# Kernel tuning notes

Measured on AMD Instinct MI355X. Metric: run time of the kernel, lower is better.

Reference implementation:

```python
import jax, jax.numpy as jnp
import numpy as np

N = 50000
E = 800000
IN_DIM, HID, HEADS, OUT = 128, 32, 8, 64
NEG_SLOPE = 0.2
EPS = 1e-16


def setup_inputs() -> dict:
    key = jax.random.key(0)
    ks = jax.random.split(key, 10)
    return {
        "x": jax.random.normal(ks[0], (N, IN_DIM), dtype=jnp.float32),
        "edge_index": jax.random.randint(ks[1], (2, E), 0, N, dtype=jnp.int64)
        if jax.config.jax_enable_x64 else jax.random.randint(ks[1], (2, E), 0, N, dtype=jnp.int32),
        "W1": jax.random.normal(ks[2], (HEADS * HID, IN_DIM), dtype=jnp.float32) * 0.1,
        "att_src1": jax.random.normal(ks[3], (HEADS, HID), dtype=jnp.float32) * 0.1,
        "att_dst1": jax.random.normal(ks[4], (HEADS, HID), dtype=jnp.float32) * 0.1,
        "b1": jnp.zeros((HEADS * HID,), dtype=jnp.float32),
        "W2": jax.random.normal(ks[5], (OUT, HEADS * HID), dtype=jnp.float32) * 0.1,
        "att_src2": jax.random.normal(ks[6], (1, OUT), dtype=jnp.float32) * 0.1,
        "att_dst2": jax.random.normal(ks[7], (1, OUT), dtype=jnp.float32) * 0.1,
        "b2": jnp.zeros((OUT,), dtype=jnp.float32),
    }


def _gat_conv(x, src, dst, W, att_src, att_dst, bias, heads, out_dim, concat, n_nodes):
    # x: [N, F_in]; W: [heads*out_dim, F_in]; att_*: [heads, out_dim]
    h = (x @ W.T).reshape(n_nodes, heads, out_dim)      # [N, H, D]
    a_src = jnp.einsum('nhd,hd->nh', h, att_src)         # [N, H]
    a_dst = jnp.einsum('nhd,hd->nh', h, att_dst)
    alpha = jax.nn.leaky_relu(a_src[src] + a_dst[dst], NEG_SLOPE)  # [E, H]
    # segment softmax over edges grouped by destination node
    m = jax.ops.segment_max(alpha, dst, num_segments=n_nodes)
    alpha = jnp.exp(alpha - m[dst])
    s = jax.ops.segment_sum(alpha, dst, num_segments=n_nodes)
    alpha = alpha / (s[dst] + EPS)
    msg = h[src] * alpha[:, :, None]                     # [E, H, D]
    out = jax.ops.segment_sum(msg, dst, num_segments=n_nodes)  # [N, H, D]
    if concat:
        out = out.reshape(n_nodes, heads * out_dim)
    else:
        out = out.mean(axis=1)
    return out + bias


def reference(x, edge_index, W1, att_src1, att_dst1, b1, W2, att_src2, att_dst2, b2):
    n = x.shape[0]
    loop = jnp.arange(n, dtype=edge_index.dtype)
    src = jnp.concatenate([edge_index[0], loop])  # PyG add_self_loops=True
    dst = jnp.concatenate([edge_index[1], loop])
    h = _gat_conv(x, src, dst, W1, att_src1, att_dst1, b1, HEADS, HID, True, n)
    h = jax.nn.relu(h)
    out = _gat_conv(h, src, dst, W2, att_src2, att_dst2, b2, 1, OUT, False, n)
    return out
```

## Files before the change

kernel.cpp:

```cpp
#include <hip/hip_runtime.h>
#include <hip/hip_fp16.h>

#define NN 50000
#define EE 800000
#define ET (EE + NN)
#define IND 128
#define F1 256
#define H1 8
#define D1 32
#define F2 64
#define NEG 0.2f
#define EPSV 1e-16f

#define MG2 391
#define SCB ((ET + 2047) / 2048)
#define BCAP 64

typedef _Float16 half8_t __attribute__((ext_vector_type(8)));
typedef float floatx4 __attribute__((ext_vector_type(4)));

#define W1N4 (256 * 128 / 4)
#define W2N4 (64 * 256 / 4)
__global__ void k_cvtW(const float* __restrict__ w1, const float* __restrict__ w2,
                       __half* __restrict__ w1p, __half* __restrict__ w2h) {
  int i = blockIdx.x * blockDim.x + threadIdx.x;
  if (i < W1N4) {
    float4 v = *(const float4*)(w1 + (size_t)i * 4);
    int col = i >> 5;
    int kb = (i * 4) & 127;
    int by = col >> 7, t = (col >> 4) & 7, ar = col & 15;
    int kk = kb >> 5, ag = (kb >> 3) & 3, j = kb & 7;
    int fid = (by * 8 + t) * 4 + kk;
    int lane = ag * 16 + ar;
    __half2 p0 = __floats2half2_rn(v.x, v.y);
    __half2 p1 = __floats2half2_rn(v.z, v.w);
    float2 st;
    *(__half2*)&st.x = p0;
    *(__half2*)&st.y = p1;
    *(float2*)(w1p + fid * 512 + lane * 8 + j) = st;
    return;
  }
  i -= W1N4;
  if (i >= W2N4) return;
  float4 v = *(const float4*)(w2 + (size_t)i * 4);
  __half2 p0 = __floats2half2_rn(v.x, v.y);
  __half2 p1 = __floats2half2_rn(v.z, v.w);
  float2 st;
  *(__half2*)&st.x = p0;
  *(__half2*)&st.y = p1;
  *(float2*)(w2h + (size_t)i * 4) = st;
}

__global__ __launch_bounds__(256) void k_scg1(const int* __restrict__ ei,
    int* __restrict__ deg, unsigned short* __restrict__ bkt,
    const float* __restrict__ A, const __half* __restrict__ Bp,
    __half* __restrict__ Ch, const float* __restrict__ as1w,
    const float* __restrict__ ad1w, float* __restrict__ as1,
    float* __restrict__ ad1) {
  if (blockIdx.x >= 2 * MG2) {
    int base = (blockIdx.x - 2 * MG2) * 2048 + threadIdx.x * 8;
    if (base >= ET) return;
    if (base + 8 <= EE) {
      int4 s0 = *(const int4*)(ei + base);
      int4 s1 = *(const int4*)(ei + base + 4);
      int4 d0 = *(const int4*)(ei + EE + base);
      int4 d1 = *(const int4*)(ei + EE + base + 4);
      int s[8] = {s0.x, s0.y, s0.z, s0.w, s1.x, s1.y, s1.z, s1.w};
      int d[8] = {d0.x, d0.y, d0.z, d0.w, d1.x, d1.y, d1.z, d1.w};
#pragma unroll
      for (int j = 0; j < 8; ++j) {
        int pos = atomicAdd(&deg[d[j]], 1);
        if (pos < BCAP) bkt[(d[j] << 6) + pos] = (unsigned short)s[j];
      }
    } else {
      for (int j = 0; j < 8; ++j) {
        int e = base + j;
        if (e >= ET) break;
        int ss, dd;
        if (e < EE) { ss = ei[e]; dd = ei[EE + e]; }
        else        { ss = e - EE; dd = ss; }
        int pos = atomicAdd(&deg[dd], 1);
        if (pos < BCAP) bkt[(dd << 6) + pos] = (unsigned short)ss;
      }
    }
    return;
  }
  int bx = blockIdx.x % MG2, by = blockIdx.x / MG2;
  int tid = threadIdx.x;
  int wv = tid >> 6, lane = tid & 63;
  int m0 = bx * 128 + wv * 16;
  int ar = lane & 15, ag = lane >> 4;
  int r0 = m0 + ar;       if (r0 >= NN) r0 = NN - 1;
  int r1 = m0 + 64 + ar;  if (r1 >= NN) r1 = NN - 1;
  const float* A0 = A + (size_t)r0 * IND + ag * 8;
  const float* A1 = A + (size_t)r1 * IND + ag * 8;
  floatx4 acc[2][8];
#pragma unroll
  for (int rt = 0; rt < 2; ++rt)
#pragma unroll
    for (int t = 0; t < 8; ++t) acc[rt][t] = (floatx4){0.f, 0.f, 0.f, 0.f};
#pragma unroll
  for (int kk = 0; kk < 4; ++kk) {
    int k0 = kk * 32;
    float4 a00 = *(const float4*)(A0 + k0);
    float4 a01 = *(const float4*)(A0 + k0 + 4);
    float4 a10 = *(const float4*)(A1 + k0);
    float4 a11 = *(const float4*)(A1 + k0 + 4);
    half8_t af0, af1;
    af0[0] = (_Float16)a00.x; af0[1] = (_Float16)a00.y;
    af0[2] = (_Float16)a00.z; af0[3] = (_Float16)a00.w;
    af0[4] = (_Float16)a01.x; af0[5] = (_Float16)a01.y;
    af0[6] = (_Float16)a01.z; af0[7] = (_Float16)a01.w;
    af1[0] = (_Float16)a10.x; af1[1] = (_Float16)a10.y;
    af1[2] = (_Float16)a10.z; af1[3] = (_Float16)a10.w;
    af1[4] = (_Float16)a11.x; af1[5] = (_Float16)a11.y;
    af1[6] = (_Float16)a11.z; af1[7] = (_Float16)a11.w;
#pragma unroll
    for (int t = 0; t < 8; ++t) {
      int fid = (by * 8 + t) * 4 + kk;
      half8_t bf = *(const half8_t*)(Bp + fid * 512 + lane * 8);
      acc[0][t] = __builtin_amdgcn_mfma_f32_16x16x32_f16(af0, bf, acc[0][t], 0, 0, 0);
      acc[1][t] = __builtin_amdgcn_mfma_f32_16x16x32_f16(af1, bf, acc[1][t], 0, 0, 0);
    }
  }
#pragma unroll
  for (int rt = 0; rt < 2; ++rt)
#pragma unroll
    for (int t = 0; t < 8; ++t) {
      int col = by * 128 + t * 16 + ar;
#pragma unroll
      for (int r = 0; r < 4; ++r) {
        int m = m0 + rt * 64 + ag * 4 + r;
        if (m < NN) Ch[(size_t)m * F1 + col] = __float2half(acc[rt][t][r]);
      }
    }
#pragma unroll
  for (int hp = 0; hp < 4; ++hp) {
    int head = by * 4 + hp;
    float sp[2][4] = {}, dp[2][4] = {};
#pragma unroll
    for (int th = 0; th < 2; ++th) {
      int t = 2 * hp + th;
      float ws = as1w[head * D1 + th * 16 + ar];
      float wd = ad1w[head * D1 + th * 16 + ar];
#pragma unroll
      for (int rt = 0; rt < 2; ++rt)
#pragma unroll
        for (int r = 0; r < 4; ++r) {
          sp[rt][r] = fmaf(acc[rt][t][r], ws, sp[rt][r]);
          dp[rt][r] = fmaf(acc[rt][t][r], wd, dp[rt][r]);
        }
    }
#pragma unroll
    for (int msk = 1; msk < 16; msk <<= 1)
#pragma unroll
      for (int rt = 0; rt < 2; ++rt)
#pragma unroll
        for (int r = 0; r < 4; ++r) {
          sp[rt][r] += __shfl_xor(sp[rt][r], msk);
          dp[rt][r] += __shfl_xor(dp[rt][r], msk);
        }
    if (ar == 0) {
#pragma unroll
      for (int rt = 0; rt < 2; ++rt)
#pragma unroll
        for (int r = 0; r < 4; ++r) {
          int m = m0 + rt * 64 + ag * 4 + r;
          if (m < NN) {
            as1[m * 8 + head] = sp[rt][r];
            ad1[m * 8 + head] = dp[rt][r];
          }
        }
    }
  }
}

__global__ __launch_bounds__(256) void k_agg1(const int* __restrict__ deg,
    const unsigned short* __restrict__ bkt, const __half* __restrict__ feat,
    const float* __restrict__ as_, const float* __restrict__ ad_,
    const float* __restrict__ bias, __half* __restrict__ outh) {
  int wid = threadIdx.x >> 6;
  int lane = threadIdx.x & 63;
  int d = blockIdx.x * 4 + wid;
  if (d >= NN) return;
  const int b = lane >> 5;
  const int q = lane & 31;
  const int h = q >> 2;
  const int sw = lane >> 3;
  const int hw = lane & 7;
  const char* fb = (const char*)feat;
  float adw = ad_[d * 8 + hw];
  float acc[8] = {};
  float wsacc = 0.f;
  int p0 = d << 6;
  int dg = deg[d];
  int p1 = p0 + dg;
  int nfull = dg >> 3;
  int p = p0;
  for (int it = 0; it < nfull; ++it, p += 8) {
    int sW = bkt[p + sw];
    float t = as_[sW * 8 + hw] + adw;
    t = (t > 0.f) ? t : NEG * t;
    float w = __expf(t);
    wsacc += w;
    int wbits = __float_as_int(w);
#pragma unroll
    for (int i = 0; i < 4; ++i) {
      int slot = 2 * i + b;
      int se = __builtin_amdgcn_ds_bpermute(slot * 32, sW);
      float wv = __int_as_float(
          __builtin_amdgcn_ds_bpermute((slot * 8 + h) * 4, wbits));
      half8_t f = *(const half8_t*)(fb + ((se << 9) | (q << 4)));
#pragma unroll
      for (int j = 0; j < 8; ++j) acc[j] = fmaf(wv, (float)f[j], acc[j]);
    }
  }
  if (p < p1) {
    int pw = p + sw;
    bool v = pw < p1;
    int sW = bkt[v ? pw : (p1 - 1)];
    float t = as_[sW * 8 + hw] + adw;
    t = (t > 0.f) ? t : NEG * t;
    float w = v ? __expf(t) : 0.f;
    wsacc += w;
    int wbits = __float_as_int(w);
#pragma unroll
    for (int i = 0; i < 4; ++i) {
      int slot = 2 * i + b;
      int se = __builtin_amdgcn_ds_bpermute(slot * 32, sW);
      float wv = __int_as_float(
          __builtin_amdgcn_ds_bpermute((slot * 8 + h) * 4, wbits));
      half8_t f = *(const half8_t*)(fb + ((se << 9) | (q << 4)));
#pragma unroll
      for (int j = 0; j < 8; ++j) acc[j] = fmaf(wv, (float)f[j], acc[j]);
    }
  }
  wsacc += __shfl_xor(wsacc, 8);
  wsacc += __shfl_xor(wsacc, 16);
  wsacc += __shfl_xor(wsacc, 32);
  float wst = __int_as_float(
      __builtin_amdgcn_ds_bpermute(h * 4, __float_as_int(wsacc)));
#pragma unroll
  for (int j = 0; j < 8; ++j) acc[j] += __shfl_xor(acc[j], 32);
  if (b == 0) {
    float inv = 1.f / (wst + EPSV);
    __half2 packs[4];
#pragma unroll
    for (int j = 0; j < 8; j += 2) {
      float o0 = fmaxf(fmaf(acc[j], inv, 0.f) + bias[q * 8 + j], 0.f);
      float o1 = fmaxf(fmaf(acc[j + 1], inv, 0.f) + bias[q * 8 + j + 1], 0.f);
      packs[j >> 1] = __floats2half2_rn(o0, o1);
    }
    *(float4*)(outh + (size_t)d * 256 + q * 8) = *(float4*)packs;
  }
}

__global__ __launch_bounds__(256) void k_g2att(const __half* __restrict__ A,
    const __half* __restrict__ Bh, __half* __restrict__ Ch,
    const float* __restrict__ as2w, const float* __restrict__ ad2w,
    float* __restrict__ as2, float* __restrict__ ad2) {
  __shared__ __half Bs[64][256 + 8];
  int tid = threadIdx.x;
  const float4* src = (const float4*)Bh;
  for (int i = tid; i < 64 * 256 / 8; i += 256) {
    int row = i / 32, kc = i % 32;
    *(float4*)&Bs[row][kc * 8] = src[i];
  }
  __syncthreads();
  int wv = tid >> 6, lane = tid & 63;
  int m0 = blockIdx.x * 128 + wv * 16;
  int ar = lane & 15, ag = lane >> 4;
  int r0 = m0 + ar;       if (r0 >= NN) r0 = NN - 1;
  int r1 = m0 + 64 + ar;  if (r1 >= NN) r1 = NN - 1;
  const __half* A0 = A + (size_t)r0 * F1 + ag * 8;
  const __half* A1 = A + (size_t)r1 * F1 + ag * 8;
  floatx4 acc[2][4];
#pragma unroll
  for (int rt = 0; rt < 2; ++rt)
#pragma unroll
    for (int t = 0; t < 4; ++t) acc[rt][t] = (floatx4){0.f, 0.f, 0.f, 0.f};
#pragma unroll
  for (int k0 = 0; k0 < F1; k0 += 32) {
    half8_t af0 = *(const half8_t*)(A0 + k0);
    half8_t af1 = *(const half8_t*)(A1 + k0);
#pragma unroll
    for (int t = 0; t < 4; ++t) {
      half8_t bf = *(const half8_t*)&Bs[t * 16 + ar][k0 + ag * 8];
      acc[0][t] = __builtin_amdgcn_mfma_f32_16x16x32_f16(af0, bf, acc[0][t], 0, 0, 0);
      acc[1][t] = __builtin_amdgcn_mfma_f32_16x16x32_f16(af1, bf, acc[1][t], 0, 0, 0);
    }
  }
  float sp[2][4] = {}, dp[2][4] = {};
#pragma unroll
  for (int t = 0; t < 4; ++t) {
    int col = t * 16 + ar;
    float ws = as2w[col], wd = ad2w[col];
#pragma unroll
    for (int rt = 0; rt < 2; ++rt)
#pragma unroll
      for (int r = 0; r < 4; ++r) {
        int m = m0 + rt * 64 + ag * 4 + r;
        if (m < NN) Ch[(size_t)m * F2 + col] = __float2half(acc[rt][t][r]);
        sp[rt][r] = fmaf(acc[rt][t][r], ws, sp[rt][r]);
        dp[rt][r] = fmaf(acc[rt][t][r], wd, dp[rt][r]);
      }
  }
#pragma unroll
  for (int msk = 1; msk < 16; msk <<= 1)
#pragma unroll
    for (int rt = 0; rt < 2; ++rt)
#pragma unroll
      for (int r = 0; r < 4; ++r) {
        sp[rt][r] += __shfl_xor(sp[rt][r], msk);
        dp[rt][r] += __shfl_xor(dp[rt][r], msk);
      }
  if (ar == 0) {
#pragma unroll
    for (int rt = 0; rt < 2; ++rt)
#pragma unroll
      for (int r = 0; r < 4; ++r) {
        int m = m0 + rt * 64 + ag * 4 + r;
        if (m < NN) { as2[m] = sp[rt][r]; ad2[m] = dp[rt][r]; }
      }
  }
}

__global__ __launch_bounds__(256) void k_agg2(const int* __restrict__ deg,
    const unsigned short* __restrict__ bkt, const __half* __restrict__ feat,
    const float* __restrict__ as_, const float* __restrict__ ad_,
    const float* __restrict__ bias, float* __restrict__ out) {
  int wid = threadIdx.x >> 6;
  int lane = threadIdx.x & 63;
  int d = blockIdx.x * 4 + wid;
  if (d >= NN) return;
  const int b = lane >> 3;
  const int q = lane & 7;
  const char* fb = (const char*)feat;
  float adv = ad_[d];
  float acc[8] = {};
  float ws = 0.f;
  int p0 = d << 6;
  int dg = deg[d];
  int p1 = p0 + dg;
  int nfull = dg >> 3;
  int p = p0;
  for (int it = 0; it < nfull; ++it, p += 8) {
    int se = bkt[p + b];
    float t = as_[se] + adv;
    t = (t > 0.f) ? t : NEG * t;
    float w = __expf(t);
    ws += w;
    half8_t f = *(const half8_t*)(fb + ((se << 7) | (q << 4)));
#pragma unroll
    for (int j = 0; j < 8; ++j) acc[j] = fmaf(w, (float)f[j], acc[j]);
  }
  if (p < p1) {
    int pe = p + b;
    bool v = pe < p1;
    int se = bkt[v ? pe : (p1 - 1)];
    float t = as_[se] + adv;
    t = (t > 0.f) ? t : NEG * t;
    float w = v ? __expf(t) : 0.f;
    ws += w;
    half8_t f = *(const half8_t*)(fb + ((se << 7) | (q << 4)));
#pragma unroll
    for (int j = 0; j < 8; ++j) acc[j] = fmaf(w, (float)f[j], acc[j]);
  }
  ws += __shfl_xor(ws, 8);
  ws += __shfl_xor(ws, 16);
  ws += __shfl_xor(ws, 32);
#pragma unroll
  for (int j = 0; j < 8; ++j) {
    acc[j] += __shfl_xor(acc[j], 8);
    acc[j] += __shfl_xor(acc[j], 16);
    acc[j] += __shfl_xor(acc[j], 32);
  }
  if (b == 0) {
    float inv = 1.f / (ws + EPSV);
    float o[8];
#pragma unroll
    for (int j = 0; j < 8; ++j) o[j] = acc[j] * inv + bias[q * 8 + j];
    *(float4*)(out + (size_t)d * 64 + q * 8) = *(float4*)&o[0];
    *(float4*)(out + (size_t)d * 64 + q * 8 + 4) = *(float4*)&o[4];
  }
}

extern "C" void kernel_launch(void* const* d_in, const int* in_sizes, int n_in,
                              void* d_out, int out_size, void* d_ws, size_t ws_size,
                              hipStream_t stream) {
  const float* x    = (const float*)d_in[0];
  const int*   ei   = (const int*)d_in[1];
  const float* W1   = (const float*)d_in[2];
  const float* as1w = (const float*)d_in[3];
  const float* ad1w = (const float*)d_in[4];
  const float* b1   = (const float*)d_in[5];
  const float* W2   = (const float*)d_in[6];
  const float* as2w = (const float*)d_in[7];
  const float* ad2w = (const float*)d_in[8];
  const float* b2   = (const float*)d_in[9];
  float* out = (float*)d_out;

  char* W = (char*)d_ws;
  __half* h1h = (__half*)W; W += (size_t)NN * 256 * 2;
  __half* h2h = (__half*)W; W += (size_t)NN * 256 * 2;
  __half* hmh = (__half*)W; W += (size_t)NN * 64 * 2;
  __half* W1p = (__half*)W; W += 256 * 128 * 2;
  __half* W2h = (__half*)W; W += 64 * 256 * 2;
  float* as1 = (float*)W; W += (size_t)NN * 8 * 4;
  float* ad1 = (float*)W; W += (size_t)NN * 8 * 4;
  float* as2 = (float*)W; W += (size_t)NN * 4;
  float* ad2 = (float*)W; W += (size_t)NN * 4;
  int* deg    = (int*)W;  W += (size_t)NN * 4;
  unsigned short* bkt = (unsigned short*)W; W += (size_t)NN * BCAP * 2;

  hipMemsetAsync(deg, 0, NN * sizeof(int), stream);

  k_cvtW<<<(W1N4 + W2N4 + 255) / 256, 256, 0, stream>>>(W1, W2, W1p, W2h);
  k_scg1<<<2 * MG2 + SCB, 256, 0, stream>>>(ei, deg, bkt, x, W1p, h1h,
                                            as1w, ad1w, as1, ad1);
  k_agg1<<<(NN + 3) / 4, 256, 0, stream>>>(deg, bkt, h1h, as1, ad1, b1, h2h);
  k_g2att<<<MG2, 256, 0, stream>>>(h2h, W2h, hmh, as2w, ad2w, as2, ad2);
  k_agg2<<<(NN + 3) / 4, 256, 0, stream>>>(deg, bkt, hmh, as2, ad2, b2, out);
}
```

Measured before the change: 177.9 us.

## Partition edge bucketing by destination range per XCD and fold deg memset

New measurement: 178.1 us. No clear change (+0.2%).

```diff
diff --git a/kernel.cpp b/kernel.cpp
--- a/kernel.cpp
+++ b/kernel.cpp
@@ -14,6 +14,8 @@
 
 #define MG2 391
 #define SCB ((ET + 2047) / 2048)
+#define NXCD 8
+#define DPX (NN / NXCD)
 #define BCAP 64
 
 typedef _Float16 half8_t __attribute__((ext_vector_type(8)));
@@ -21,8 +23,11 @@
 
 #define W1N4 (256 * 128 / 4)
 #define W2N4 (64 * 256 / 4)
+#define DEG4 (NN / 4)
+#define CVTN (W1N4 + W2N4 + DEG4)
 __global__ void k_cvtW(const float* __restrict__ w1, const float* __restrict__ w2,
-                       __half* __restrict__ w1p, __half* __restrict__ w2h) {
+                       __half* __restrict__ w1p, __half* __restrict__ w2h,
+                       int* __restrict__ deg) {
   int i = blockIdx.x * blockDim.x + threadIdx.x;
   if (i < W1N4) {
     float4 v = *(const float4*)(w1 + (size_t)i * 4);
@@ -41,14 +46,21 @@
     return;
   }
   i -= W1N4;
-  if (i >= W2N4) return;
-  float4 v = *(const float4*)(w2 + (size_t)i * 4);
-  __half2 p0 = __floats2half2_rn(v.x, v.y);
-  __half2 p1 = __floats2half2_rn(v.z, v.w);
-  float2 st;
-  *(__half2*)&st.x = p0;
-  *(__half2*)&st.y = p1;
-  *(float2*)(w2h + (size_t)i * 4) = st;
+  if (i < W2N4) {
+    float4 v = *(const float4*)(w2 + (size_t)i * 4);
+    __half2 p0 = __floats2half2_rn(v.x, v.y);
+    __half2 p1 = __floats2half2_rn(v.z, v.w);
+    float2 st;
+    *(__half2*)&st.x = p0;
+    *(__half2*)&st.y = p1;
+    *(float2*)(w2h + (size_t)i * 4) = st;
+    return;
+  }
+  i -= W2N4;
+  if (i < DEG4) {
+    int4 z = make_int4(0, 0, 0, 0);
+    *(int4*)(deg + i * 4) = z;
+  }
 }
 
 __global__ __launch_bounds__(256) void k_scg1(const int* __restrict__ ei,
@@ -58,7 +70,11 @@
     const float* __restrict__ ad1w, float* __restrict__ as1,
     float* __restrict__ ad1) {
   if (blockIdx.x >= 2 * MG2) {
-    int base = (blockIdx.x - 2 * MG2) * 2048 + threadIdx.x * 8;
+    int sb = blockIdx.x - 2 * MG2;
+    int cls = sb & 7;
+    int chunk = sb >> 3;
+    int lo = cls * DPX, hi = lo + DPX;
+    int base = chunk * 2048 + threadIdx.x * 8;
     if (base >= ET) return;
     if (base + 8 <= EE) {
       int4 s0 = *(const int4*)(ei + base);
@@ -69,8 +85,10 @@
       int d[8] = {d0.x, d0.y, d0.z, d0.w, d1.x, d1.y, d1.z, d1.w};
 #pragma unroll
       for (int j = 0; j < 8; ++j) {
-        int pos = atomicAdd(&deg[d[j]], 1);
-        if (pos < BCAP) bkt[(d[j] << 6) + pos] = (unsigned short)s[j];
+        if (d[j] >= lo && d[j] < hi) {
+          int pos = atomicAdd(&deg[d[j]], 1);
+          if (pos < BCAP) bkt[(d[j] << 6) + pos] = (unsigned short)s[j];
+        }
       }
     } else {
       for (int j = 0; j < 8; ++j) {
@@ -79,8 +97,10 @@
         int ss, dd;
         if (e < EE) { ss = ei[e]; dd = ei[EE + e]; }
         else        { ss = e - EE; dd = ss; }
-        int pos = atomicAdd(&deg[dd], 1);
-        if (pos < BCAP) bkt[(dd << 6) + pos] = (unsigned short)ss;
+        if (dd >= lo && dd < hi) {
+          int pos = atomicAdd(&deg[dd], 1);
+          if (pos < BCAP) bkt[(dd << 6) + pos] = (unsigned short)ss;
+        }
       }
     }
     return;
@@ -413,11 +433,9 @@
   int* deg    = (int*)W;  W += (size_t)NN * 4;
   unsigned short* bkt = (unsigned short*)W; W += (size_t)NN * BCAP * 2;
 
-  hipMemsetAsync(deg, 0, NN * sizeof(int), stream);
-
-  k_cvtW<<<(W1N4 + W2N4 + 255) / 256, 256, 0, stream>>>(W1, W2, W1p, W2h);
-  k_scg1<<<2 * MG2 + SCB, 256, 0, stream>>>(ei, deg, bkt, x, W1p, h1h,
-                                            as1w, ad1w, as1, ad1);
+  k_cvtW<<<(CVTN + 255) / 256, 256, 0, stream>>>(W1, W2, W1p, W2h, deg);
+  k_scg1<<<2 * MG2 + NXCD * SCB, 256, 0, stream>>>(ei, deg, bkt, x, W1p, h1h,
+                                                   as1w, ad1w, as1, ad1);
   k_agg1<<<(NN + 3) / 4, 256, 0, stream>>>(deg, bkt, h1h, as1, ad1, b1, h2h);
   k_g2att<<<MG2, 256, 0, stream>>>(h2h, W2h, hmh, as2w, ad2w, as2, ad2);
   k_agg2<<<(NN + 3) / 4, 256, 0, stream>>>(deg, bkt, hmh, as2, ad2, b2, out);
```

## Fuse layer-2 linear and attention logits into layer-1 aggregation; fold degree memset

Applied to the files above, without the earlier changes.

New measurement: 313.1 us. 1.76x slower.

```diff
diff --git a/kernel.cpp b/kernel.cpp
--- a/kernel.cpp
+++ b/kernel.cpp
@@ -21,8 +21,11 @@
 
 #define W1N4 (256 * 128 / 4)
 #define W2N4 (64 * 256 / 4)
+#define DEG4 (NN / 4)
+#define CVTN (W1N4 + W2N4 + DEG4)
 __global__ void k_cvtW(const float* __restrict__ w1, const float* __restrict__ w2,
-                       __half* __restrict__ w1p, __half* __restrict__ w2h) {
+                       __half* __restrict__ w1p, __half* __restrict__ w2h,
+                       int* __restrict__ deg) {
   int i = blockIdx.x * blockDim.x + threadIdx.x;
   if (i < W1N4) {
     float4 v = *(const float4*)(w1 + (size_t)i * 4);
@@ -41,14 +44,21 @@
     return;
   }
   i -= W1N4;
-  if (i >= W2N4) return;
-  float4 v = *(const float4*)(w2 + (size_t)i * 4);
-  __half2 p0 = __floats2half2_rn(v.x, v.y);
-  __half2 p1 = __floats2half2_rn(v.z, v.w);
-  float2 st;
-  *(__half2*)&st.x = p0;
-  *(__half2*)&st.y = p1;
-  *(float2*)(w2h + (size_t)i * 4) = st;
+  if (i < W2N4) {
+    float4 v = *(const float4*)(w2 + (size_t)i * 4);
+    __half2 p0 = __floats2half2_rn(v.x, v.y);
+    __half2 p1 = __floats2half2_rn(v.z, v.w);
+    float2 st;
+    *(__half2*)&st.x = p0;
+    *(__half2*)&st.y = p1;
+    *(float2*)(w2h + (size_t)i * 4) = st;
+    return;
+  }
+  i -= W2N4;
+  if (i < DEG4) {
+    int4 z = make_int4(0, 0, 0, 0);
+    *(int4*)(deg + i * 4) = z;
+  }
 }
 
 __global__ __launch_bounds__(256) void k_scg1(const int* __restrict__ ei,
@@ -178,11 +188,13 @@
 __global__ __launch_bounds__(256) void k_agg1(const int* __restrict__ deg,
     const unsigned short* __restrict__ bkt, const __half* __restrict__ feat,
     const float* __restrict__ as_, const float* __restrict__ ad_,
-    const float* __restrict__ bias, __half* __restrict__ outh) {
+    const float* __restrict__ bias, const __half* __restrict__ W2h,
+    const float* __restrict__ as2w, const float* __restrict__ ad2w,
+    __half* __restrict__ hmh, float* __restrict__ as2, float* __restrict__ ad2) {
+  __shared__ __half h2s[4][256];
   int wid = threadIdx.x >> 6;
   int lane = threadIdx.x & 63;
   int d = blockIdx.x * 4 + wid;
-  if (d >= NN) return;
   const int b = lane >> 5;
   const int q = lane & 31;
   const int h = q >> 2;
@@ -242,7 +254,7 @@
       __builtin_amdgcn_ds_bpermute(h * 4, __float_as_int(wsacc)));
 #pragma unroll
   for (int j = 0; j < 8; ++j) acc[j] += __shfl_xor(acc[j], 32);
-  if (b == 0) {
+  {
     float inv = 1.f / (wst + EPSV);
     __half2 packs[4];
 #pragma unroll
@@ -251,78 +263,28 @@
       float o1 = fmaxf(fmaf(acc[j + 1], inv, 0.f) + bias[q * 8 + j + 1], 0.f);
       packs[j >> 1] = __floats2half2_rn(o0, o1);
     }
-    *(float4*)(outh + (size_t)d * 256 + q * 8) = *(float4*)packs;
-  }
-}
-
-__global__ __launch_bounds__(256) void k_g2att(const __half* __restrict__ A,
-    const __half* __restrict__ Bh, __half* __restrict__ Ch,
-    const float* __restrict__ as2w, const float* __restrict__ ad2w,
-    float* __restrict__ as2, float* __restrict__ ad2) {
-  __shared__ __half Bs[64][256 + 8];
-  int tid = threadIdx.x;
-  const float4* src = (const float4*)Bh;
-  for (int i = tid; i < 64 * 256 / 8; i += 256) {
-    int row = i / 32, kc = i % 32;
-    *(float4*)&Bs[row][kc * 8] = src[i];
+    if (b == 0) *(float4*)&h2s[wid][q * 8] = *(float4*)packs;
   }
   __syncthreads();
-  int wv = tid >> 6, lane = tid & 63;
-  int m0 = blockIdx.x * 128 + wv * 16;
-  int ar = lane & 15, ag = lane >> 4;
-  int r0 = m0 + ar;       if (r0 >= NN) r0 = NN - 1;
-  int r1 = m0 + 64 + ar;  if (r1 >= NN) r1 = NN - 1;
-  const __half* A0 = A + (size_t)r0 * F1 + ag * 8;
-  const __half* A1 = A + (size_t)r1 * F1 + ag * 8;
-  floatx4 acc[2][4];
-#pragma unroll
-  for (int rt = 0; rt < 2; ++rt)
-#pragma unroll
-    for (int t = 0; t < 4; ++t) acc[rt][t] = (floatx4){0.f, 0.f, 0.f, 0.f};
-#pragma unroll
-  for (int k0 = 0; k0 < F1; k0 += 32) {
-    half8_t af0 = *(const half8_t*)(A0 + k0);
-    half8_t af1 = *(const half8_t*)(A1 + k0);
-#pragma unroll
-    for (int t = 0; t < 4; ++t) {
-      half8_t bf = *(const half8_t*)&Bs[t * 16 + ar][k0 + ag * 8];
-      acc[0][t] = __builtin_amdgcn_mfma_f32_16x16x32_f16(af0, bf, acc[0][t], 0, 0, 0);
-      acc[1][t] = __builtin_amdgcn_mfma_f32_16x16x32_f16(af1, bf, acc[1][t], 0, 0, 0);
-    }
-  }
-  float sp[2][4] = {}, dp[2][4] = {};
-#pragma unroll
-  for (int t = 0; t < 4; ++t) {
-    int col = t * 16 + ar;
-    float ws = as2w[col], wd = ad2w[col];
-#pragma unroll
-    for (int rt = 0; rt < 2; ++rt)
-#pragma unroll
-      for (int r = 0; r < 4; ++r) {
-        int m = m0 + rt * 64 + ag * 4 + r;
-        if (m < NN) Ch[(size_t)m * F2 + col] = __float2half(acc[rt][t][r]);
-        sp[rt][r] = fmaf(acc[rt][t][r], ws, sp[rt][r]);
-        dp[rt][r] = fmaf(acc[rt][t][r], wd, dp[rt][r]);
-      }
-  }
-#pragma unroll
-  for (int msk = 1; msk < 16; msk <<= 1)
-#pragma unroll
-    for (int rt = 0; rt < 2; ++rt)
-#pragma unroll
-      for (int r = 0; r < 4; ++r) {
-        sp[rt][r] += __shfl_xor(sp[rt][r], msk);
-        dp[rt][r] += __shfl_xor(dp[rt][r], msk);
-      }
-  if (ar == 0) {
-#pragma unroll
-    for (int rt = 0; rt < 2; ++rt)
-#pragma unroll
-      for (int r = 0; r < 4; ++r) {
-        int m = m0 + rt * 64 + ag * 4 + r;
-        if (m < NN) { as2[m] = sp[rt][r]; ad2[m] = dp[rt][r]; }
-      }
-  }
+  const __half* wrow = W2h + lane * 256;
+  float acc2 = 0.f;
+#pragma unroll
+  for (int k0 = 0; k0 < 256; k0 += 8) {
+    half8_t hv = *(const half8_t*)&h2s[wid][k0];
+    half8_t wv = *(const half8_t*)(wrow + k0);
+#pragma unroll
+    for (int j = 0; j < 8; ++j)
+      acc2 = fmaf((float)hv[j], (float)wv[j], acc2);
+  }
+  hmh[(size_t)d * 64 + lane] = __float2half(acc2);
+  float s2 = acc2 * as2w[lane];
+  float d2 = acc2 * ad2w[lane];
+#pragma unroll
+  for (int m = 1; m < 64; m <<= 1) {
+    s2 += __shfl_xor(s2, m);
+    d2 += __shfl_xor(d2, m);
+  }
+  if (lane == 0) { as2[d] = s2; ad2[d] = d2; }
 }
 
 __global__ __launch_bounds__(256) void k_agg2(const int* __restrict__ deg,
@@ -402,7 +364,6 @@
 
   char* W = (char*)d_ws;
   __half* h1h = (__half*)W; W += (size_t)NN * 256 * 2;
-  __half* h2h = (__half*)W; W += (size_t)NN * 256 * 2;
   __half* hmh = (__half*)W; W += (size_t)NN * 64 * 2;
   __half* W1p = (__half*)W; W += 256 * 128 * 2;
   __half* W2h = (__half*)W; W += 64 * 256 * 2;
@@ -413,12 +374,10 @@
   int* deg    = (int*)W;  W += (size_t)NN * 4;
   unsigned short* bkt = (unsigned short*)W; W += (size_t)NN * BCAP * 2;
 
-  hipMemsetAsync(deg, 0, NN * sizeof(int), stream);
-
-  k_cvtW<<<(W1N4 + W2N4 + 255) / 256, 256, 0, stream>>>(W1, W2, W1p, W2h);
+  k_cvtW<<<(CVTN + 255) / 256, 256, 0, stream>>>(W1, W2, W1p, W2h, deg);
   k_scg1<<<2 * MG2 + SCB, 256, 0, stream>>>(ei, deg, bkt, x, W1p, h1h,
                                             as1w, ad1w, as1, ad1);
-  k_agg1<<<(NN + 3) / 4, 256, 0, stream>>>(deg, bkt, h1h, as1, ad1, b1, h2h);
-  k_g2att<<<MG2, 256, 0, stream>>>(h2h, W2h, hmh, as2w, ad2w, as2, ad2);
+  k_agg1<<<(NN + 3) / 4, 256, 0, stream>>>(deg, bkt, h1h, as1, ad1, b1,
+                                           W2h, as2w, ad2w, hmh, as2, ad2);
   k_agg2<<<(NN + 3) / 4, 256, 0, stream>>>(deg, bkt, hmh, as2, ad2, b2, out);
 }
```

## Fold layer-2 attention projections into agg1 and split agg2 across feature halves

Applied to the files above, without the earlier changes.

Result: slower. 195.4 us (+9.9%).

```diff
diff --git a/kernel.cpp b/kernel.cpp
--- a/kernel.cpp
+++ b/kernel.cpp
@@ -17,12 +17,18 @@
 #define BCAP 64
 
 typedef _Float16 half8_t __attribute__((ext_vector_type(8)));
+typedef _Float16 half4_t __attribute__((ext_vector_type(4)));
 typedef float floatx4 __attribute__((ext_vector_type(4)));
 
 #define W1N4 (256 * 128 / 4)
 #define W2N4 (64 * 256 / 4)
+#define DEG4 (NN / 4)
+#define CVTN (W1N4 + W2N4 + DEG4 + 256)
 __global__ void k_cvtW(const float* __restrict__ w1, const float* __restrict__ w2,
-                       __half* __restrict__ w1p, __half* __restrict__ w2h) {
+                       __half* __restrict__ w1p, __half* __restrict__ w2h,
+                       int* __restrict__ deg, const float* __restrict__ as2w,
+                       const float* __restrict__ ad2w, float* __restrict__ v2s,
+                       float* __restrict__ v2d) {
   int i = blockIdx.x * blockDim.x + threadIdx.x;
   if (i < W1N4) {
     float4 v = *(const float4*)(w1 + (size_t)i * 4);
@@ -41,14 +47,34 @@
     return;
   }
   i -= W1N4;
-  if (i >= W2N4) return;
-  float4 v = *(const float4*)(w2 + (size_t)i * 4);
-  __half2 p0 = __floats2half2_rn(v.x, v.y);
-  __half2 p1 = __floats2half2_rn(v.z, v.w);
-  float2 st;
-  *(__half2*)&st.x = p0;
-  *(__half2*)&st.y = p1;
-  *(float2*)(w2h + (size_t)i * 4) = st;
+  if (i < W2N4) {
+    float4 v = *(const float4*)(w2 + (size_t)i * 4);
+    __half2 p0 = __floats2half2_rn(v.x, v.y);
+    __half2 p1 = __floats2half2_rn(v.z, v.w);
+    float2 st;
+    *(__half2*)&st.x = p0;
+    *(__half2*)&st.y = p1;
+    *(float2*)(w2h + (size_t)i * 4) = st;
+    return;
+  }
+  i -= W2N4;
+  if (i < DEG4) {
+    int4 z = make_int4(0, 0, 0, 0);
+    *(int4*)(deg + i * 4) = z;
+    return;
+  }
+  i -= DEG4;
+  if (i < 256) {
+    float s = 0.f, d = 0.f;
+#pragma unroll 8
+    for (int c = 0; c < 64; ++c) {
+      float w = w2[c * 256 + i];
+      s = fmaf(w, as2w[c], s);
+      d = fmaf(w, ad2w[c], d);
+    }
+    v2s[i] = s;
+    v2d[i] = d;
+  }
 }
 
 __global__ __launch_bounds__(256) void k_scg1(const int* __restrict__ ei,
@@ -178,7 +204,9 @@
 __global__ __launch_bounds__(256) void k_agg1(const int* __restrict__ deg,
     const unsigned short* __restrict__ bkt, const __half* __restrict__ feat,
     const float* __restrict__ as_, const float* __restrict__ ad_,
-    const float* __restrict__ bias, __half* __restrict__ outh) {
+    const float* __restrict__ bias, const float* __restrict__ v2s,
+    const float* __restrict__ v2d, __half* __restrict__ outh,
+    float* __restrict__ as2, float* __restrict__ ad2) {
   int wid = threadIdx.x >> 6;
   int lane = threadIdx.x & 63;
   int d = blockIdx.x * 4 + wid;
@@ -242,23 +270,34 @@
       __builtin_amdgcn_ds_bpermute(h * 4, __float_as_int(wsacc)));
 #pragma unroll
   for (int j = 0; j < 8; ++j) acc[j] += __shfl_xor(acc[j], 32);
+  float inv = 1.f / (wst + EPSV);
+  float o[8];
+#pragma unroll
+  for (int j = 0; j < 8; ++j)
+    o[j] = fmaxf(fmaf(acc[j], inv, 0.f) + bias[q * 8 + j], 0.f);
   if (b == 0) {
-    float inv = 1.f / (wst + EPSV);
     __half2 packs[4];
 #pragma unroll
-    for (int j = 0; j < 8; j += 2) {
-      float o0 = fmaxf(fmaf(acc[j], inv, 0.f) + bias[q * 8 + j], 0.f);
-      float o1 = fmaxf(fmaf(acc[j + 1], inv, 0.f) + bias[q * 8 + j + 1], 0.f);
-      packs[j >> 1] = __floats2half2_rn(o0, o1);
-    }
+    for (int j = 0; j < 8; j += 2)
+      packs[j >> 1] = __floats2half2_rn(o[j], o[j + 1]);
     *(float4*)(outh + (size_t)d * 256 + q * 8) = *(float4*)packs;
   }
-}
-
-__global__ __launch_bounds__(256) void k_g2att(const __half* __restrict__ A,
-    const __half* __restrict__ Bh, __half* __restrict__ Ch,
-    const float* __restrict__ as2w, const float* __restrict__ ad2w,
-    float* __restrict__ as2, float* __restrict__ ad2) {
+  float s2 = 0.f, d2 = 0.f;
+#pragma unroll
+  for (int j = 0; j < 8; ++j) {
+    s2 = fmaf(o[j], v2s[q * 8 + j], s2);
+    d2 = fmaf(o[j], v2d[q * 8 + j], d2);
+  }
+#pragma unroll
+  for (int m = 1; m < 64; m <<= 1) {
+    s2 += __shfl_xor(s2, m);
+    d2 += __shfl_xor(d2, m);
+  }
+  if (lane == 0) { as2[d] = 0.5f * s2; ad2[d] = 0.5f * d2; }
+}
+
+__global__ __launch_bounds__(256) void k_g2(const __half* __restrict__ A,
+    const __half* __restrict__ Bh, __half* __restrict__ Ch) {
   __shared__ __half Bs[64][256 + 8];
   int tid = threadIdx.x;
   const float4* src = (const float4*)Bh;
@@ -290,54 +329,34 @@
       acc[1][t] = __builtin_amdgcn_mfma_f32_16x16x32_f16(af1, bf, acc[1][t], 0, 0, 0);
     }
   }
-  float sp[2][4] = {}, dp[2][4] = {};
-#pragma unroll
-  for (int t = 0; t < 4; ++t) {
-    int col = t * 16 + ar;
-    float ws = as2w[col], wd = ad2w[col];
-#pragma unroll
-    for (int rt = 0; rt < 2; ++rt)
+#pragma unroll
+  for (int rt = 0; rt < 2; ++rt)
+#pragma unroll
+    for (int t = 0; t < 4; ++t) {
+      int col = t * 16 + ar;
 #pragma unroll
       for (int r = 0; r < 4; ++r) {
         int m = m0 + rt * 64 + ag * 4 + r;
         if (m < NN) Ch[(size_t)m * F2 + col] = __float2half(acc[rt][t][r]);
-        sp[rt][r] = fmaf(acc[rt][t][r], ws, sp[rt][r]);
-        dp[rt][r] = fmaf(acc[rt][t][r], wd, dp[rt][r]);
       }
-  }
-#pragma unroll
-  for (int msk = 1; msk < 16; msk <<= 1)
-#pragma unroll
-    for (int rt = 0; rt < 2; ++rt)
-#pragma unroll
-      for (int r = 0; r < 4; ++r) {
-        sp[rt][r] += __shfl_xor(sp[rt][r], msk);
-        dp[rt][r] += __shfl_xor(dp[rt][r], msk);
-      }
-  if (ar == 0) {
-#pragma unroll
-    for (int rt = 0; rt < 2; ++rt)
-#pragma unroll
-      for (int r = 0; r < 4; ++r) {
-        int m = m0 + rt * 64 + ag * 4 + r;
-        if (m < NN) { as2[m] = sp[rt][r]; ad2[m] = dp[rt][r]; }
-      }
-  }
+    }
 }
 
 __global__ __launch_bounds__(256) void k_agg2(const int* __restrict__ deg,
     const unsigned short* __restrict__ bkt, const __half* __restrict__ feat,
     const float* __restrict__ as_, const float* __restrict__ ad_,
     const float* __restrict__ bias, float* __restrict__ out) {
+  int slice = blockIdx.x & 1;
+  int chunk = blockIdx.x >> 1;
   int wid = threadIdx.x >> 6;
   int lane = threadIdx.x & 63;
-  int d = blockIdx.x * 4 + wid;
+  int d = chunk * 4 + wid;
   if (d >= NN) return;
   const int b = lane >> 3;
   const int q = lane & 7;
-  const char* fb = (const char*)feat;
+  const char* fb = (const char*)feat + (slice << 6);
   float adv = ad_[d];
-  float acc[8] = {};
+  float a0 = 0.f, a1 = 0.f, a2 = 0.f, a3 = 0.f;
   float ws = 0.f;
   int p0 = d << 6;
   int dg = deg[d];
@@ -350,9 +369,11 @@
     t = (t > 0.f) ? t : NEG * t;
     float w = __expf(t);
     ws += w;
-    half8_t f = *(const half8_t*)(fb + ((se << 7) | (q << 4)));
-#pragma unroll
-    for (int j = 0; j < 8; ++j) acc[j] = fmaf(w, (float)f[j], acc[j]);
+    half4_t f = *(const half4_t*)(fb + ((se << 7) | (q << 3)));
+    a0 = fmaf(w, (float)f[0], a0);
+    a1 = fmaf(w, (float)f[1], a1);
+    a2 = fmaf(w, (float)f[2], a2);
+    a3 = fmaf(w, (float)f[3], a3);
   }
   if (p < p1) {
     int pe = p + b;
@@ -362,26 +383,26 @@
     t = (t > 0.f) ? t : NEG * t;
     float w = v ? __expf(t) : 0.f;
     ws += w;
-    half8_t f = *(const half8_t*)(fb + ((se << 7) | (q << 4)));
-#pragma unroll
-    for (int j = 0; j < 8; ++j) acc[j] = fmaf(w, (float)f[j], acc[j]);
-  }
-  ws += __shfl_xor(ws, 8);
-  ws += __shfl_xor(ws, 16);
-  ws += __shfl_xor(ws, 32);
-#pragma unroll
-  for (int j = 0; j < 8; ++j) {
-    acc[j] += __shfl_xor(acc[j], 8);
-    acc[j] += __shfl_xor(acc[j], 16);
-    acc[j] += __shfl_xor(acc[j], 32);
-  }
+    half4_t f = *(const half4_t*)(fb + ((se << 7) | (q << 3)));
+    a0 = fmaf(w, (float)f[0], a0);
+    a1 = fmaf(w, (float)f[1], a1);
+    a2 = fmaf(w, (float)f[2], a2);
+    a3 = fmaf(w, (float)f[3], a3);
+  }
+  ws += __shfl_xor(ws, 8); ws += __shfl_xor(ws, 16); ws += __shfl_xor(ws, 32);
+  a0 += __shfl_xor(a0, 8); a0 += __shfl_xor(a0, 16); a0 += __shfl_xor(a0, 32);
+  a1 += __shfl_xor(a1, 8); a1 += __shfl_xor(a1, 16); a1 += __shfl_xor(a1, 32);
+  a2 += __shfl_xor(a2, 8); a2 += __shfl_xor(a2, 16); a2 += __shfl_xor(a2, 32);
+  a3 += __shfl_xor(a3, 8); a3 += __shfl_xor(a3, 16); a3 += __shfl_xor(a3, 32);
   if (b == 0) {
     float inv = 1.f / (ws + EPSV);
-    float o[8];
-#pragma unroll
-    for (int j = 0; j < 8; ++j) o[j] = acc[j] * inv + bias[q * 8 + j];
-    *(float4*)(out + (size_t)d * 64 + q * 8) = *(float4*)&o[0];
-    *(float4*)(out + (size_t)d * 64 + q * 8 + 4) = *(float4*)&o[4];
+    int d0 = slice * 32 + q * 4;
+    float4 o;
+    o.x = fmaf(a0, inv, bias[d0 + 0]);
+    o.y = fmaf(a1, inv, bias[d0 + 1]);
+    o.z = fmaf(a2, inv, bias[d0 + 2]);
+    o.w = fmaf(a3, inv, bias[d0 + 3]);
+    *(float4*)(out + (size_t)d * 64 + d0) = o;
   }
 }
 
@@ -410,15 +431,17 @@
   float* ad1 = (float*)W; W += (size_t)NN * 8 * 4;
   float* as2 = (float*)W; W += (size_t)NN * 4;
   float* ad2 = (float*)W; W += (size_t)NN * 4;
+  float* v2s = (float*)W; W += 256 * 4;
+  float* v2d = (float*)W; W += 256 * 4;
   int* deg    = (int*)W;  W += (size_t)NN * 4;
   unsigned short* bkt = (unsigned short*)W; W += (size_t)NN * BCAP * 2;
 
-  hipMemsetAsync(deg, 0, NN * sizeof(int), stream);
-
-  k_cvtW<<<(W1N4 + W2N4 + 255) / 256, 256, 0, stream>>>(W1, W2, W1p, W2h);
+  k_cvtW<<<(CVTN + 255) / 256, 256, 0, stream>>>(W1, W2, W1p, W2h, deg,
+                                                 as2w, ad2w, v2s, v2d);
   k_scg1<<<2 * MG2 + SCB, 256, 0, stream>>>(ei, deg, bkt, x, W1p, h1h,
                                             as1w, ad1w, as1, ad1);
-  k_agg1<<<(NN + 3) / 4, 256, 0, stream>>>(deg, bkt, h1h, as1, ad1, b1, h2h);
-  k_g2att<<<MG2, 256, 0, stream>>>(h2h, W2h, hmh, as2w, ad2w, as2, ad2);
-  k_agg2<<<(NN + 3) / 4, 256, 0, stream>>>(deg, bkt, hmh, as2, ad2, b2, out);
-}
+  k_agg1<<<(NN + 3) / 4, 256, 0, stream>>>(deg, bkt, h1h, as1, ad1, b1,
+                                           v2s, v2d, h2h, as2, ad2);
+  k_g2<<<MG2, 256, 0, stream>>>(h2h, W2h, hmh);
+  k_agg2<<<2 * ((NN + 3) / 4), 256, 0, stream>>>(deg, bkt, hmh, as2, ad2, b2, out);
+}
```
